# Optimization experiments

Hardware: AMD Instinct MI355X
Metric: run time of the kernel (lower is better)

Reference implementation:

```python
import jax, jax.numpy as jnp
import numpy as np

N, T, C, K = 32, 1024, 512, 64
EPS = 1e-12  # torch F.normalize eps


def _l2norm(v, axis):
    n = jnp.sqrt(jnp.sum(v * v, axis=axis, keepdims=True))
    return v / jnp.maximum(n, EPS)


def setup_inputs() -> dict:
    key = jax.random.key(0)
    k1, k2 = jax.random.split(key)
    x = jax.random.normal(k1, (N, T, C), dtype=jnp.float32)
    centroids = jax.random.uniform(k2, (K, C), dtype=jnp.float32)
    # mirrors _init_params: conv.weight = 0.2*centroids, conv.bias = -0.1*||centroids||
    W = 0.2 * centroids
    b = -0.1 * jnp.sqrt(jnp.sum(centroids * centroids, axis=1))
    return {"x": x, "W": W, "b": b, "centroids": centroids}


def reference(x, W, b, centroids):
    # x: [N, T, C] -> [N, C, T]
    xt = jnp.transpose(x, (0, 2, 1))
    # 1x1 Conv1d == per-timestep linear: logits [N, K, T]
    logits = jnp.einsum('kc,nct->nkt', W, xt) + b[None, :, None]
    a = jax.nn.softmax(logits, axis=1)  # softmax over clusters
    # vlad[n,k,c] = sum_t a[n,k,t] * (x[n,c,t] - centroid[k,c])
    #            = (a @ x^T) - sum_t(a) * centroid  (GEMM form, same math)
    vlad = jnp.einsum('nkt,nct->nkc', a, xt) - a.sum(axis=-1)[:, :, None] * centroids[None]
    vlad = _l2norm(vlad, axis=2)          # intra-normalization per cluster
    vlad = vlad.reshape(vlad.shape[0], -1)
    vlad = _l2norm(vlad, axis=1)          # global L2 normalization
    return vlad
```

## Files before the change

### kernel.cpp

```cpp
#include <hip/hip_runtime.h>
#include <cmath>

namespace {

constexpr int N = 32, T = 1024, C = 512, K = 64;
constexpr float EPS = 1e-12f;

typedef __attribute__((ext_vector_type(8))) short s8v;
typedef __attribute__((ext_vector_type(4))) short s4v;
typedef __attribute__((ext_vector_type(4))) float f4v;

__device__ inline unsigned short f2bh(float f) {
  __bf16 h = (__bf16)f;
  return __builtin_bit_cast(unsigned short, h);
}
__device__ inline float bh2f(unsigned short u) {
  __bf16 h = __builtin_bit_cast(__bf16, u);
  return (float)h;
}

#define MFMA16(A, B, Cc) __builtin_amdgcn_mfma_f32_16x16x32_bf16((A), (B), (Cc), 0, 0, 0)

__global__ __launch_bounds__(256) void k_prep(const float* __restrict__ W,
                                              unsigned short* __restrict__ Wh,
                                              unsigned short* __restrict__ Wl) {
  const int f = blockIdx.x * 256 + threadIdx.x;
  const float4 w = *(const float4*)&W[f * 4];
  float e[4] = {w.x, w.y, w.z, w.w};
  s4v h, l;
#pragma unroll
  for (int i = 0; i < 4; ++i) {
    unsigned short hb = f2bh(e[i]);
    h[i] = (short)hb;
    l[i] = (short)f2bh(e[i] - bh2f(hb));
  }
  *(s4v*)&Wh[f * 4] = h;
  *(s4v*)&Wl[f * 4] = l;
}

__global__ __launch_bounds__(512, 4) void k_gemm1(
    const float* __restrict__ x, const unsigned short* __restrict__ Wh,
    const unsigned short* __restrict__ Wl, const float* __restrict__ b,
    unsigned short* __restrict__ ath, unsigned short* __restrict__ atl,
    float* __restrict__ asum) {
  __shared__ __align__(16) unsigned short sm[4 * 64 * 72];
  __shared__ float asum_l[64];
  unsigned short* xh_s = sm;
  unsigned short* xl_s = sm + 64 * 72;
  unsigned short* wh_s = sm + 2 * 64 * 72;
  unsigned short* wl_s = sm + 3 * 64 * 72;

  const int tid = threadIdx.x;
  const int w = tid >> 6, lane = tid & 63, lm = lane & 15, lq = lane >> 4;
  const int tt = w >> 1;
  const int kh = w & 1;
  const long r0 = (long)blockIdx.x * 64;
  const int n = blockIdx.x >> 4;
  const int tl0 = (blockIdx.x & 15) * 64;

  if (tid < 64) asum_l[tid] = 0.f;

  f4v acc0 = {0.f, 0.f, 0.f, 0.f}, acc1 = {0.f, 0.f, 0.f, 0.f};
  const float bias0 = b[kh * 32 + lm], bias1 = b[kh * 32 + 16 + lm];

  for (int c0 = 0; c0 < C; c0 += 64) {
#pragma unroll
    for (int rr = 0; rr < 2; ++rr) {
      const int f = tid + rr * 512, t = f >> 4, cg = f & 15;
      const float4 xv = *(const float4*)&x[(r0 + t) * C + c0 + cg * 4];
      float e[4] = {xv.x, xv.y, xv.z, xv.w};
      s4v h, l;
#pragma unroll
      for (int i = 0; i < 4; ++i) {
        unsigned short hb = f2bh(e[i]);
        h[i] = (short)hb;
        l[i] = (short)f2bh(e[i] - bh2f(hb));
      }
      *(s4v*)&xh_s[t * 72 + cg * 4] = h;
      *(s4v*)&xl_s[t * 72 + cg * 4] = l;
    }
    {
      const int k = tid >> 3, u = tid & 7;
      *(s8v*)&wh_s[k * 72 + u * 8] = *(const s8v*)&Wh[k * C + c0 + u * 8];
      *(s8v*)&wl_s[k * 72 + u * 8] = *(const s8v*)&Wl[k * C + c0 + u * 8];
    }
    __syncthreads();

#pragma unroll
    for (int ks = 0; ks < 2; ++ks) {
      const int col = ks * 32 + lq * 8;
      const s8v ah = *(const s8v*)&xh_s[(tt * 16 + lm) * 72 + col];
      const s8v al = *(const s8v*)&xl_s[(tt * 16 + lm) * 72 + col];
      const s8v bh0 = *(const s8v*)&wh_s[(kh * 32 + lm) * 72 + col];
      const s8v bh1 = *(const s8v*)&wh_s[(kh * 32 + 16 + lm) * 72 + col];
      const s8v bl0 = *(const s8v*)&wl_s[(kh * 32 + lm) * 72 + col];
      const s8v bl1 = *(const s8v*)&wl_s[(kh * 32 + 16 + lm) * 72 + col];
      acc0 = MFMA16(ah, bh0, acc0);
      acc0 = MFMA16(ah, bl0, acc0);
      acc0 = MFMA16(al, bh0, acc0);
      acc1 = MFMA16(ah, bh1, acc1);
      acc1 = MFMA16(ah, bl1, acc1);
      acc1 = MFMA16(al, bh1, acc1);
    }
    __syncthreads();
  }

  float* Ls = (float*)sm;
  unsigned short* ath_l = sm + 8704;
  unsigned short* atl_l = sm + 8704 + 4864;
#pragma unroll
  for (int r = 0; r < 4; ++r) {
    Ls[(tt * 16 + lq * 4 + r) * 68 + kh * 32 + lm] = acc0[r] + bias0;
    Ls[(tt * 16 + lq * 4 + r) * 68 + kh * 32 + 16 + lm] = acc1[r] + bias1;
  }
  __syncthreads();

  {
    const int r = tid >> 3, j = tid & 7;
    const float4 v0 = *(const float4*)&Ls[r * 68 + j * 8];
    const float4 v1 = *(const float4*)&Ls[r * 68 + j * 8 + 4];
    float a[8] = {v0.x, v0.y, v0.z, v0.w, v1.x, v1.y, v1.z, v1.w};
    float m = a[0];
#pragma unroll
    for (int i = 1; i < 8; ++i) m = fmaxf(m, a[i]);
#pragma unroll
    for (int s = 1; s < 8; s <<= 1) m = fmaxf(m, __shfl_xor(m, s, 64));
    float sum = 0.f;
#pragma unroll
    for (int i = 0; i < 8; ++i) {
      a[i] = __expf(a[i] - m);
      sum += a[i];
    }
#pragma unroll
    for (int s = 1; s < 8; s <<= 1) sum += __shfl_xor(sum, s, 64);
    const float inv = 1.f / sum;
    float ps[8];
#pragma unroll
    for (int i = 0; i < 8; ++i) {
      a[i] *= inv;
      ps[i] = a[i];
    }
#pragma unroll
    for (int s = 8; s < 64; s <<= 1)
#pragma unroll
      for (int i = 0; i < 8; ++i) ps[i] += __shfl_xor(ps[i], s, 64);
    if ((tid & 56) == 0) {
#pragma unroll
      for (int i = 0; i < 8; ++i) atomicAdd(&asum_l[j * 8 + i], ps[i]);
    }
#pragma unroll
    for (int i = 0; i < 8; ++i) {
      const unsigned short hb = f2bh(a[i]);
      ath_l[(j * 8 + i) * 76 + r] = hb;
      atl_l[(j * 8 + i) * 76 + r] = f2bh(a[i] - bh2f(hb));
    }
  }
  __syncthreads();

  if (tid < 64) atomicAdd(&asum[n * K + tid], asum_l[tid]);
#pragma unroll
  for (int m = 0; m < 4; ++m) {
    const int idx = tid + m * 512;
    const int sel = idx >> 10, rem = idx & 1023, k = rem >> 4, uu = rem & 15;
    const unsigned short* src = sel ? atl_l : ath_l;
    unsigned short* dst = sel ? atl : ath;
    *(s4v*)&dst[((long)n * K + k) * T + tl0 + uu * 4] =
        *(const s4v*)&src[k * 76 + uu * 4];
  }
}

__global__ __launch_bounds__(256, 4) void k_gemm2(
    const float* __restrict__ x, const unsigned short* __restrict__ ath,
    const unsigned short* __restrict__ atl, float* __restrict__ part, int TS) {
  __shared__ __align__(16) unsigned short sm[4 * 64 * 72];
  unsigned short* ah_s = sm;
  unsigned short* al_s = sm + 4608;
  unsigned short* xh_s = sm + 9216;
  unsigned short* xl_s = sm + 13824;

  const int tid = threadIdx.x;
  const int w = tid >> 6, lane = tid & 63, lm = lane & 15, lq = lane >> 4;
  const int kh = w >> 1;
  const int ch = w & 1;
  const int bi = blockIdx.x;
  const int cchunk = bi & 7;
  const int tmp = bi >> 3;
  const int tchunk = tmp % TS, n = tmp / TS;
  const int c0 = cchunk * 64;
  const int tlen = T / TS;

  f4v acc[2][2] = {{{0.f, 0.f, 0.f, 0.f}, {0.f, 0.f, 0.f, 0.f}},
                   {{0.f, 0.f, 0.f, 0.f}, {0.f, 0.f, 0.f, 0.f}}};

  for (int t0 = tchunk * tlen; t0 < tchunk * tlen + tlen; t0 += 64) {
#pragma unroll
    for (int m = 0; m < 4; ++m) {
      const int idx = tid + m * 256;
      const int sel = idx >> 9, rem = idx & 511, k = rem >> 3, u = rem & 7;
      const unsigned short* src = sel ? atl : ath;
      unsigned short* dst = sel ? al_s : ah_s;
      *(s8v*)&dst[k * 72 + u * 8] =
          *(const s8v*)&src[((long)n * K + k) * T + t0 + u * 8];
    }
    {
      const int cg = tid & 15, tq = tid >> 4, t4 = tq * 4;
      float e[4][4];
#pragma unroll
      for (int i = 0; i < 4; ++i) {
        const float4 v =
            *(const float4*)&x[((long)n * T + t0 + t4 + i) * C + c0 + cg * 4];
        e[i][0] = v.x; e[i][1] = v.y; e[i][2] = v.z; e[i][3] = v.w;
      }
#pragma unroll
      for (int cc = 0; cc < 4; ++cc) {
        s4v h, l;
#pragma unroll
        for (int i = 0; i < 4; ++i) {
          unsigned short hb = f2bh(e[i][cc]);
          h[i] = (short)hb;
          l[i] = (short)f2bh(e[i][cc] - bh2f(hb));
        }
        *(s4v*)&xh_s[(cg * 4 + cc) * 72 + t4] = h;
        *(s4v*)&xl_s[(cg * 4 + cc) * 72 + t4] = l;
      }
    }
    __syncthreads();

#pragma unroll
    for (int ks = 0; ks < 2; ++ks) {
      const int col = ks * 32 + lq * 8;
      const s8v ah0 = *(const s8v*)&ah_s[(kh * 32 + lm) * 72 + col];
      const s8v ah1 = *(const s8v*)&ah_s[(kh * 32 + 16 + lm) * 72 + col];
      const s8v al0 = *(const s8v*)&al_s[(kh * 32 + lm) * 72 + col];
      const s8v al1 = *(const s8v*)&al_s[(kh * 32 + 16 + lm) * 72 + col];
      const s8v bh0 = *(const s8v*)&xh_s[(ch * 32 + lm) * 72 + col];
      const s8v bh1 = *(const s8v*)&xh_s[(ch * 32 + 16 + lm) * 72 + col];
      const s8v bl0 = *(const s8v*)&xl_s[(ch * 32 + lm) * 72 + col];
      const s8v bl1 = *(const s8v*)&xl_s[(ch * 32 + 16 + lm) * 72 + col];
      acc[0][0] = MFMA16(ah0, bh0, acc[0][0]);
      acc[0][0] = MFMA16(ah0, bl0, acc[0][0]);
      acc[0][0] = MFMA16(al0, bh0, acc[0][0]);
      acc[0][1] = MFMA16(ah0, bh1, acc[0][1]);
      acc[0][1] = MFMA16(ah0, bl1, acc[0][1]);
      acc[0][1] = MFMA16(al0, bh1, acc[0][1]);
      acc[1][0] = MFMA16(ah1, bh0, acc[1][0]);
      acc[1][0] = MFMA16(ah1, bl0, acc[1][0]);
      acc[1][0] = MFMA16(al1, bh0, acc[1][0]);
      acc[1][1] = MFMA16(ah1, bh1, acc[1][1]);
      acc[1][1] = MFMA16(ah1, bl1, acc[1][1]);
      acc[1][1] = MFMA16(al1, bh1, acc[1][1]);
    }
    __syncthreads();
  }

  float* pbase = part + ((long)tchunk * N + n) * K * C;
#pragma unroll
  for (int mt = 0; mt < 2; ++mt)
#pragma unroll
    for (int nt = 0; nt < 2; ++nt)
#pragma unroll
      for (int r = 0; r < 4; ++r) {
        const int k = kh * 32 + mt * 16 + lq * 4 + r;
        const int c = c0 + ch * 32 + nt * 16 + lm;
        pbase[(long)k * C + c] = acc[mt][nt][r];
      }
}

__global__ __launch_bounds__(128) void k_reduce(
    const float* __restrict__ part, const float* __restrict__ asum,
    const float* __restrict__ cent, float* __restrict__ vlad,
    float* __restrict__ sumsq, int TS) {
  __shared__ float r2[2];
  const int tid = threadIdx.x;
  const int n = blockIdx.x >> 6;
  const int k = blockIdx.x & 63;
  const int c = tid * 4;

  float4 v = {0.f, 0.f, 0.f, 0.f};
  for (int p = 0; p < TS; ++p) {
    const float4 pv =
        *(const float4*)&part[(((long)p * N + n) * K + k) * C + c];
    v.x += pv.x; v.y += pv.y; v.z += pv.z; v.w += pv.w;
  }
  const float as = asum[n * K + k];
  const float4 cv = *(const float4*)&cent[(long)k * C + c];
  v.x -= as * cv.x; v.y -= as * cv.y; v.z -= as * cv.z; v.w -= as * cv.w;
  *(float4*)&vlad[((long)n * K + k) * C + c] = v;

  float ss = v.x * v.x + v.y * v.y + v.z * v.z + v.w * v.w;
#pragma unroll
  for (int s = 1; s < 64; s <<= 1) ss += __shfl_xor(ss, s, 64);
  if ((tid & 63) == 0) r2[tid >> 6] = ss;
  __syncthreads();
  if (tid == 0) sumsq[n * K + k] = r2[0] + r2[1];
}

__global__ __launch_bounds__(256) void k_norm(
    const float* __restrict__ vlad, const float* __restrict__ sumsq,
    float* __restrict__ out) {
  __shared__ float denom[64];
  __shared__ float contrib[64];
  __shared__ float ginv;

  const int tid = threadIdx.x;
  const int n = blockIdx.x >> 4;
  const int chunk = blockIdx.x & 15;

  if (tid < 64) {
    const float ss = sumsq[n * K + tid];
    const float d = fmaxf(sqrtf(ss), EPS);
    denom[tid] = d;
    contrib[tid] = ss / (d * d);
  }
  __syncthreads();
  if (tid == 0) {
    float s = 0.f;
#pragma unroll
    for (int k = 0; k < K; ++k) s += contrib[k];
    ginv = 1.0f / fmaxf(sqrtf(s), EPS);
  }
  __syncthreads();

#pragma unroll
  for (int q = 0; q < 2; ++q) {
    const int f4 = tid + q * 256;
    const long off = chunk * 2048 + (long)f4 * 4;
    const int k = (int)(off >> 9);
    float4 v = *(const float4*)&vlad[(long)n * K * C + off];
    const float sc = ginv / denom[k];
    v.x *= sc; v.y *= sc; v.z *= sc; v.w *= sc;
    *(float4*)&out[(long)n * K * C + off] = v;
  }
}

}

extern "C" void kernel_launch(void* const* d_in, const int* in_sizes, int n_in,
                              void* d_out, int out_size, void* d_ws,
                              size_t ws_size, hipStream_t stream) {
  const float* x = reinterpret_cast<const float*>(d_in[0]);
  const float* W = reinterpret_cast<const float*>(d_in[1]);
  const float* b = reinterpret_cast<const float*>(d_in[2]);
  const float* cent = reinterpret_cast<const float*>(d_in[3]);
  float* out = reinterpret_cast<float*>(d_out);

  const size_t AT_BYTES = (size_t)N * K * T * 2;
  const size_t PART1 = (size_t)N * K * C * 4;
  const size_t W_BYTES = (size_t)K * C * 2;
  const size_t TAIL = 2 * W_BYTES + 2 * 8192;

  int TS = 4;
  while (TS > 1 && 2 * AT_BYTES + (size_t)TS * PART1 + TAIL > ws_size) TS >>= 1;

  char* p = (char*)d_ws;
  unsigned short* ath = (unsigned short*)p;        p += AT_BYTES;
  unsigned short* atl = (unsigned short*)p;        p += AT_BYTES;
  float* part = (float*)p;                         p += (size_t)TS * PART1;
  unsigned short* Wh = (unsigned short*)p;         p += W_BYTES;
  unsigned short* Wl = (unsigned short*)p;         p += W_BYTES;
  float* asum = (float*)p;                         p += 8192;
  float* sumsq = (float*)p;
  float* vlad = (float*)ath;

  hipMemsetAsync(asum, 0, (size_t)N * K * sizeof(float), stream);

  k_prep<<<32, 256, 0, stream>>>(W, Wh, Wl);
  k_gemm1<<<(N * T) / 64, 512, 0, stream>>>(x, Wh, Wl, b, ath, atl, asum);
  k_gemm2<<<N * TS * 8, 256, 0, stream>>>(x, ath, atl, part, TS);
  k_reduce<<<N * K, 128, 0, stream>>>(part, asum, cent, vlad, sumsq, TS);
  k_norm<<<N * 16, 256, 0, stream>>>(vlad, sumsq, out);
}
```

Before: 146.4 us.

## Restructure VLAD GEMMs with register prefetch, larger tiles, and fp32 assignment buffer

Removes the W pre-split kernel and the memset. gemm1 now splits W into bf16 hi/lo parts inline, and its 256 threads each compute 2x2 MFMA tiles. Both GEMMs prefetch the next global tile into registers while the current one is converted and computed. The soft-assignment is stored once as fp32 and split in gemm2, whose tile grows to 64x128 (fewer blocks, launch bound of 2). Cluster sums go to per-block partial buffers reduced in k_reduce instead of atomics; this trades more register pressure and lower occupancy for fewer launches, fewer syncs and more operand reuse.

```diff
diff --git a/kernel.cpp b/kernel.cpp
--- a/kernel.cpp
+++ b/kernel.cpp
@@ -6,9 +6,9 @@
 constexpr int N = 32, T = 1024, C = 512, K = 64;
 constexpr float EPS = 1e-12f;
 
-typedef __attribute__((ext_vector_type(8))) short s8v;
-typedef __attribute__((ext_vector_type(4))) short s4v;
-typedef __attribute__((ext_vector_type(4))) float f4v;
+typedef short s8v __attribute__((ext_vector_type(8)));
+typedef short s4v __attribute__((ext_vector_type(4)));
+typedef float f4v __attribute__((ext_vector_type(4)));
 
 __device__ inline unsigned short f2bh(float f) {
   __bf16 h = (__bf16)f;
@@ -21,30 +21,12 @@
 
 #define MFMA16(A, B, Cc) __builtin_amdgcn_mfma_f32_16x16x32_bf16((A), (B), (Cc), 0, 0, 0)
 
-__global__ __launch_bounds__(256) void k_prep(const float* __restrict__ W,
-                                              unsigned short* __restrict__ Wh,
-                                              unsigned short* __restrict__ Wl) {
-  const int f = blockIdx.x * 256 + threadIdx.x;
-  const float4 w = *(const float4*)&W[f * 4];
-  float e[4] = {w.x, w.y, w.z, w.w};
-  s4v h, l;
-#pragma unroll
-  for (int i = 0; i < 4; ++i) {
-    unsigned short hb = f2bh(e[i]);
-    h[i] = (short)hb;
-    l[i] = (short)f2bh(e[i] - bh2f(hb));
-  }
-  *(s4v*)&Wh[f * 4] = h;
-  *(s4v*)&Wl[f * 4] = l;
-}
-
-__global__ __launch_bounds__(512, 4) void k_gemm1(
-    const float* __restrict__ x, const unsigned short* __restrict__ Wh,
-    const unsigned short* __restrict__ Wl, const float* __restrict__ b,
-    unsigned short* __restrict__ ath, unsigned short* __restrict__ atl,
-    float* __restrict__ asum) {
+__global__ __launch_bounds__(256, 4) void k_gemm1(
+    const float* __restrict__ x, const float* __restrict__ W,
+    const float* __restrict__ b, float* __restrict__ aT,
+    float* __restrict__ asum_part) {
   __shared__ __align__(16) unsigned short sm[4 * 64 * 72];
-  __shared__ float asum_l[64];
+  __shared__ float asum_l[256];
   unsigned short* xh_s = sm;
   unsigned short* xl_s = sm + 64 * 72;
   unsigned short* wh_s = sm + 2 * 64 * 72;
@@ -52,163 +34,195 @@
 
   const int tid = threadIdx.x;
   const int w = tid >> 6, lane = tid & 63, lm = lane & 15, lq = lane >> 4;
-  const int tt = w >> 1;
+  const int th = w >> 1;
   const int kh = w & 1;
   const long r0 = (long)blockIdx.x * 64;
-  const int n = blockIdx.x >> 4;
-  const int tl0 = (blockIdx.x & 15) * 64;
-
-  if (tid < 64) asum_l[tid] = 0.f;
-
-  f4v acc0 = {0.f, 0.f, 0.f, 0.f}, acc1 = {0.f, 0.f, 0.f, 0.f};
-  const float bias0 = b[kh * 32 + lm], bias1 = b[kh * 32 + 16 + lm];
+  const int n = blockIdx.x >> 4, tl = blockIdx.x & 15;
+
+  f4v acc[2][2] = {};
+  float4 px[4], pw[4];
+#pragma unroll
+  for (int r = 0; r < 4; ++r) {
+    const int f = tid + r * 256, t = f >> 4, cg = f & 15;
+    px[r] = *(const float4*)&x[(r0 + t) * C + cg * 4];
+    pw[r] = *(const float4*)&W[(long)t * C + cg * 4];
+  }
 
   for (int c0 = 0; c0 < C; c0 += 64) {
-#pragma unroll
-    for (int rr = 0; rr < 2; ++rr) {
-      const int f = tid + rr * 512, t = f >> 4, cg = f & 15;
-      const float4 xv = *(const float4*)&x[(r0 + t) * C + c0 + cg * 4];
-      float e[4] = {xv.x, xv.y, xv.z, xv.w};
-      s4v h, l;
+    __syncthreads();
+#pragma unroll
+    for (int r = 0; r < 4; ++r) {
+      const int f = tid + r * 256, t = f >> 4, cg = f & 15;
+      const float ex[4] = {px[r].x, px[r].y, px[r].z, px[r].w};
+      const float ew[4] = {pw[r].x, pw[r].y, pw[r].z, pw[r].w};
+      s4v xh, xl, wh, wl;
 #pragma unroll
       for (int i = 0; i < 4; ++i) {
-        unsigned short hb = f2bh(e[i]);
-        h[i] = (short)hb;
-        l[i] = (short)f2bh(e[i] - bh2f(hb));
-      }
-      *(s4v*)&xh_s[t * 72 + cg * 4] = h;
-      *(s4v*)&xl_s[t * 72 + cg * 4] = l;
-    }
-    {
-      const int k = tid >> 3, u = tid & 7;
-      *(s8v*)&wh_s[k * 72 + u * 8] = *(const s8v*)&Wh[k * C + c0 + u * 8];
-      *(s8v*)&wl_s[k * 72 + u * 8] = *(const s8v*)&Wl[k * C + c0 + u * 8];
+        unsigned short hb = f2bh(ex[i]);
+        xh[i] = (short)hb; xl[i] = (short)f2bh(ex[i] - bh2f(hb));
+        hb = f2bh(ew[i]);
+        wh[i] = (short)hb; wl[i] = (short)f2bh(ew[i] - bh2f(hb));
+      }
+      *(s4v*)&xh_s[t * 72 + cg * 4] = xh;
+      *(s4v*)&xl_s[t * 72 + cg * 4] = xl;
+      *(s4v*)&wh_s[t * 72 + cg * 4] = wh;
+      *(s4v*)&wl_s[t * 72 + cg * 4] = wl;
+    }
+    if (c0 + 64 < C) {
+#pragma unroll
+      for (int r = 0; r < 4; ++r) {
+        const int f = tid + r * 256, t = f >> 4, cg = f & 15;
+        px[r] = *(const float4*)&x[(r0 + t) * C + c0 + 64 + cg * 4];
+        pw[r] = *(const float4*)&W[(long)t * C + c0 + 64 + cg * 4];
+      }
     }
     __syncthreads();
 
 #pragma unroll
     for (int ks = 0; ks < 2; ++ks) {
       const int col = ks * 32 + lq * 8;
-      const s8v ah = *(const s8v*)&xh_s[(tt * 16 + lm) * 72 + col];
-      const s8v al = *(const s8v*)&xl_s[(tt * 16 + lm) * 72 + col];
-      const s8v bh0 = *(const s8v*)&wh_s[(kh * 32 + lm) * 72 + col];
-      const s8v bh1 = *(const s8v*)&wh_s[(kh * 32 + 16 + lm) * 72 + col];
-      const s8v bl0 = *(const s8v*)&wl_s[(kh * 32 + lm) * 72 + col];
-      const s8v bl1 = *(const s8v*)&wl_s[(kh * 32 + 16 + lm) * 72 + col];
-      acc0 = MFMA16(ah, bh0, acc0);
-      acc0 = MFMA16(ah, bl0, acc0);
-      acc0 = MFMA16(al, bh0, acc0);
-      acc1 = MFMA16(ah, bh1, acc1);
-      acc1 = MFMA16(ah, bl1, acc1);
-      acc1 = MFMA16(al, bh1, acc1);
-    }
-    __syncthreads();
-  }
+      s8v ah[2], al[2], bh[2], bl[2];
+#pragma unroll
+      for (int i = 0; i < 2; ++i) {
+        ah[i] = *(const s8v*)&xh_s[(th * 32 + i * 16 + lm) * 72 + col];
+        al[i] = *(const s8v*)&xl_s[(th * 32 + i * 16 + lm) * 72 + col];
+        bh[i] = *(const s8v*)&wh_s[(kh * 32 + i * 16 + lm) * 72 + col];
+        bl[i] = *(const s8v*)&wl_s[(kh * 32 + i * 16 + lm) * 72 + col];
+      }
+#pragma unroll
+      for (int i = 0; i < 2; ++i)
+#pragma unroll
+        for (int j = 0; j < 2; ++j) {
+          acc[i][j] = MFMA16(ah[i], bh[j], acc[i][j]);
+          acc[i][j] = MFMA16(ah[i], bl[j], acc[i][j]);
+          acc[i][j] = MFMA16(al[i], bh[j], acc[i][j]);
+        }
+    }
+  }
+  __syncthreads();
 
   float* Ls = (float*)sm;
-  unsigned short* ath_l = sm + 8704;
-  unsigned short* atl_l = sm + 8704 + 4864;
+  float* Ls2 = (float*)(sm + 8704);
+  const float bias[2] = {b[kh * 32 + lm], b[kh * 32 + 16 + lm]};
+#pragma unroll
+  for (int i = 0; i < 2; ++i)
+#pragma unroll
+    for (int j = 0; j < 2; ++j)
+#pragma unroll
+      for (int r = 0; r < 4; ++r)
+        Ls[(th * 32 + i * 16 + lq * 4 + r) * 68 + kh * 32 + j * 16 + lm] =
+            acc[i][j][r] + bias[j];
+  __syncthreads();
+
+  {
+    const int row = tid >> 2, q = tid & 3;
+    float av[16];
+#pragma unroll
+    for (int u = 0; u < 4; ++u)
+      *(float4*)&av[u * 4] = *(const float4*)&Ls[row * 68 + q * 16 + u * 4];
+    float m = av[0];
+#pragma unroll
+    for (int i = 1; i < 16; ++i) m = fmaxf(m, av[i]);
+    m = fmaxf(m, __shfl_xor(m, 1, 64));
+    m = fmaxf(m, __shfl_xor(m, 2, 64));
+    float sum = 0.f;
+#pragma unroll
+    for (int i = 0; i < 16; ++i) {
+      av[i] = __expf(av[i] - m);
+      sum += av[i];
+    }
+    sum += __shfl_xor(sum, 1, 64);
+    sum += __shfl_xor(sum, 2, 64);
+    const float inv = 1.f / sum;
+    float ps[16];
+#pragma unroll
+    for (int i = 0; i < 16; ++i) {
+      av[i] *= inv;
+      ps[i] = av[i];
+      Ls2[(q * 16 + i) * 68 + row] = av[i];
+    }
+#pragma unroll
+    for (int s = 4; s < 64; s <<= 1)
+#pragma unroll
+      for (int i = 0; i < 16; ++i) ps[i] += __shfl_xor(ps[i], s, 64);
+    if (lane < 4) {
+#pragma unroll
+      for (int i = 0; i < 16; ++i) asum_l[w * 64 + q * 16 + i] = ps[i];
+    }
+  }
+  __syncthreads();
+
+  if (tid < 64) {
+    asum_part[(n * 16 + tl) * 64 + tid] = asum_l[tid] + asum_l[64 + tid] +
+                                          asum_l[128 + tid] + asum_l[192 + tid];
+  }
 #pragma unroll
   for (int r = 0; r < 4; ++r) {
-    Ls[(tt * 16 + lq * 4 + r) * 68 + kh * 32 + lm] = acc0[r] + bias0;
-    Ls[(tt * 16 + lq * 4 + r) * 68 + kh * 32 + 16 + lm] = acc1[r] + bias1;
-  }
-  __syncthreads();
-
-  {
-    const int r = tid >> 3, j = tid & 7;
-    const float4 v0 = *(const float4*)&Ls[r * 68 + j * 8];
-    const float4 v1 = *(const float4*)&Ls[r * 68 + j * 8 + 4];
-    float a[8] = {v0.x, v0.y, v0.z, v0.w, v1.x, v1.y, v1.z, v1.w};
-    float m = a[0];
-#pragma unroll
-    for (int i = 1; i < 8; ++i) m = fmaxf(m, a[i]);
-#pragma unroll
-    for (int s = 1; s < 8; s <<= 1) m = fmaxf(m, __shfl_xor(m, s, 64));
-    float sum = 0.f;
-#pragma unroll
-    for (int i = 0; i < 8; ++i) {
-      a[i] = __expf(a[i] - m);
-      sum += a[i];
-    }
-#pragma unroll
-    for (int s = 1; s < 8; s <<= 1) sum += __shfl_xor(sum, s, 64);
-    const float inv = 1.f / sum;
-    float ps[8];
-#pragma unroll
-    for (int i = 0; i < 8; ++i) {
-      a[i] *= inv;
-      ps[i] = a[i];
-    }
-#pragma unroll
-    for (int s = 8; s < 64; s <<= 1)
-#pragma unroll
-      for (int i = 0; i < 8; ++i) ps[i] += __shfl_xor(ps[i], s, 64);
-    if ((tid & 56) == 0) {
-#pragma unroll
-      for (int i = 0; i < 8; ++i) atomicAdd(&asum_l[j * 8 + i], ps[i]);
-    }
-#pragma unroll
-    for (int i = 0; i < 8; ++i) {
-      const unsigned short hb = f2bh(a[i]);
-      ath_l[(j * 8 + i) * 76 + r] = hb;
-      atl_l[(j * 8 + i) * 76 + r] = f2bh(a[i] - bh2f(hb));
-    }
-  }
-  __syncthreads();
-
-  if (tid < 64) atomicAdd(&asum[n * K + tid], asum_l[tid]);
-#pragma unroll
-  for (int m = 0; m < 4; ++m) {
-    const int idx = tid + m * 512;
-    const int sel = idx >> 10, rem = idx & 1023, k = rem >> 4, uu = rem & 15;
-    const unsigned short* src = sel ? atl_l : ath_l;
-    unsigned short* dst = sel ? atl : ath;
-    *(s4v*)&dst[((long)n * K + k) * T + tl0 + uu * 4] =
-        *(const s4v*)&src[k * 76 + uu * 4];
-  }
-}
-
-__global__ __launch_bounds__(256, 4) void k_gemm2(
-    const float* __restrict__ x, const unsigned short* __restrict__ ath,
-    const unsigned short* __restrict__ atl, float* __restrict__ part, int TS) {
-  __shared__ __align__(16) unsigned short sm[4 * 64 * 72];
+    const int u = tid + r * 256, k = u >> 4, tg = u & 15;
+    *(float4*)&aT[((long)n * K + k) * T + tl * 64 + tg * 4] =
+        *(const float4*)&Ls2[k * 68 + tg * 4];
+  }
+}
+
+__global__ __launch_bounds__(256, 2) void k_gemm2(
+    const float* __restrict__ x, const float* __restrict__ aT,
+    float* __restrict__ part, int TS) {
+  __shared__ __align__(16) unsigned short sm[(2 * 64 + 2 * 128) * 72];
   unsigned short* ah_s = sm;
-  unsigned short* al_s = sm + 4608;
-  unsigned short* xh_s = sm + 9216;
-  unsigned short* xl_s = sm + 13824;
+  unsigned short* al_s = sm + 64 * 72;
+  unsigned short* xh_s = sm + 2 * 64 * 72;
+  unsigned short* xl_s = sm + 2 * 64 * 72 + 128 * 72;
 
   const int tid = threadIdx.x;
   const int w = tid >> 6, lane = tid & 63, lm = lane & 15, lq = lane >> 4;
   const int kh = w >> 1;
   const int ch = w & 1;
   const int bi = blockIdx.x;
-  const int cchunk = bi & 7;
-  const int tmp = bi >> 3;
+  const int cchunk = bi & 3;
+  const int tmp = bi >> 2;
   const int tchunk = tmp % TS, n = tmp / TS;
-  const int c0 = cchunk * 64;
-  const int tlen = T / TS;
-
-  f4v acc[2][2] = {{{0.f, 0.f, 0.f, 0.f}, {0.f, 0.f, 0.f, 0.f}},
-                   {{0.f, 0.f, 0.f, 0.f}, {0.f, 0.f, 0.f, 0.f}}};
-
-  for (int t0 = tchunk * tlen; t0 < tchunk * tlen + tlen; t0 += 64) {
-#pragma unroll
-    for (int m = 0; m < 4; ++m) {
-      const int idx = tid + m * 256;
-      const int sel = idx >> 9, rem = idx & 511, k = rem >> 3, u = rem & 7;
-      const unsigned short* src = sel ? atl : ath;
-      unsigned short* dst = sel ? al_s : ah_s;
-      *(s8v*)&dst[k * 72 + u * 8] =
-          *(const s8v*)&src[((long)n * K + k) * T + t0 + u * 8];
-    }
-    {
-      const int cg = tid & 15, tq = tid >> 4, t4 = tq * 4;
+  const int c0 = cchunk * 128;
+  const int tlen = T / TS, tbase = tchunk * tlen;
+
+  f4v acc[2][4] = {};
+  float4 pa[4];
+#pragma unroll
+  for (int r = 0; r < 4; ++r) {
+    const int u = tid + r * 256, k = u >> 4, tg = u & 15;
+    pa[r] = *(const float4*)&aT[((long)n * K + k) * T + tbase + tg * 4];
+  }
+
+  for (int t0 = tbase; t0 < tbase + tlen; t0 += 64) {
+    __syncthreads();
+#pragma unroll
+    for (int r = 0; r < 4; ++r) {
+      const int u = tid + r * 256, k = u >> 4, tg = u & 15;
+      const float e[4] = {pa[r].x, pa[r].y, pa[r].z, pa[r].w};
+      s4v h, l;
+#pragma unroll
+      for (int i = 0; i < 4; ++i) {
+        unsigned short hb = f2bh(e[i]);
+        h[i] = (short)hb;
+        l[i] = (short)f2bh(e[i] - bh2f(hb));
+      }
+      *(s4v*)&ah_s[k * 72 + tg * 4] = h;
+      *(s4v*)&al_s[k * 72 + tg * 4] = l;
+    }
+    if (t0 + 64 < tbase + tlen) {
+#pragma unroll
+      for (int r = 0; r < 4; ++r) {
+        const int u = tid + r * 256, k = u >> 4, tg = u & 15;
+        pa[r] = *(const float4*)&aT[((long)n * K + k) * T + t0 + 64 + tg * 4];
+      }
+    }
+#pragma unroll
+    for (int r = 0; r < 2; ++r) {
+      const int u = tid + r * 256, cg = u & 31, tq = u >> 5;
       float e[4][4];
 #pragma unroll
       for (int i = 0; i < 4; ++i) {
         const float4 v =
-            *(const float4*)&x[((long)n * T + t0 + t4 + i) * C + c0 + cg * 4];
+            *(const float4*)&x[((long)n * T + t0 + tq * 4 + i) * C + c0 + cg * 4];
         e[i][0] = v.x; e[i][1] = v.y; e[i][2] = v.z; e[i][3] = v.w;
       }
 #pragma unroll
@@ -220,8 +234,8 @@
           h[i] = (short)hb;
           l[i] = (short)f2bh(e[i][cc] - bh2f(hb));
         }
-        *(s4v*)&xh_s[(cg * 4 + cc) * 72 + t4] = h;
-        *(s4v*)&xl_s[(cg * 4 + cc) * 72 + t4] = l;
+        *(s4v*)&xh_s[(cg * 4 + cc) * 72 + tq * 4] = h;
+        *(s4v*)&xl_s[(cg * 4 + cc) * 72 + tq * 4] = l;
       }
     }
     __syncthreads();
@@ -229,45 +243,41 @@
 #pragma unroll
     for (int ks = 0; ks < 2; ++ks) {
       const int col = ks * 32 + lq * 8;
-      const s8v ah0 = *(const s8v*)&ah_s[(kh * 32 + lm) * 72 + col];
-      const s8v ah1 = *(const s8v*)&ah_s[(kh * 32 + 16 + lm) * 72 + col];
-      const s8v al0 = *(const s8v*)&al_s[(kh * 32 + lm) * 72 + col];
-      const s8v al1 = *(const s8v*)&al_s[(kh * 32 + 16 + lm) * 72 + col];
-      const s8v bh0 = *(const s8v*)&xh_s[(ch * 32 + lm) * 72 + col];
-      const s8v bh1 = *(const s8v*)&xh_s[(ch * 32 + 16 + lm) * 72 + col];
-      const s8v bl0 = *(const s8v*)&xl_s[(ch * 32 + lm) * 72 + col];
-      const s8v bl1 = *(const s8v*)&xl_s[(ch * 32 + 16 + lm) * 72 + col];
-      acc[0][0] = MFMA16(ah0, bh0, acc[0][0]);
-      acc[0][0] = MFMA16(ah0, bl0, acc[0][0]);
-      acc[0][0] = MFMA16(al0, bh0, acc[0][0]);
-      acc[0][1] = MFMA16(ah0, bh1, acc[0][1]);
-      acc[0][1] = MFMA16(ah0, bl1, acc[0][1]);
-      acc[0][1] = MFMA16(al0, bh1, acc[0][1]);
-      acc[1][0] = MFMA16(ah1, bh0, acc[1][0]);
-      acc[1][0] = MFMA16(ah1, bl0, acc[1][0]);
-      acc[1][0] = MFMA16(al1, bh0, acc[1][0]);
-      acc[1][1] = MFMA16(ah1, bh1, acc[1][1]);
-      acc[1][1] = MFMA16(ah1, bl1, acc[1][1]);
-      acc[1][1] = MFMA16(al1, bh1, acc[1][1]);
-    }
-    __syncthreads();
-  }
-
-  float* pbase = part + ((long)tchunk * N + n) * K * C;
-#pragma unroll
-  for (int mt = 0; mt < 2; ++mt)
-#pragma unroll
-    for (int nt = 0; nt < 2; ++nt)
+      s8v ah[2], al[2];
+#pragma unroll
+      for (int i = 0; i < 2; ++i) {
+        ah[i] = *(const s8v*)&ah_s[(kh * 32 + i * 16 + lm) * 72 + col];
+        al[i] = *(const s8v*)&al_s[(kh * 32 + i * 16 + lm) * 72 + col];
+      }
+#pragma unroll
+      for (int j = 0; j < 4; ++j) {
+        const s8v bh = *(const s8v*)&xh_s[(ch * 64 + j * 16 + lm) * 72 + col];
+        const s8v bl = *(const s8v*)&xl_s[(ch * 64 + j * 16 + lm) * 72 + col];
+#pragma unroll
+        for (int i = 0; i < 2; ++i) {
+          acc[i][j] = MFMA16(ah[i], bh, acc[i][j]);
+          acc[i][j] = MFMA16(ah[i], bl, acc[i][j]);
+          acc[i][j] = MFMA16(al[i], bh, acc[i][j]);
+        }
+      }
+    }
+  }
+
+  float* pb = part + ((long)tchunk * N + n) * K * C;
+#pragma unroll
+  for (int i = 0; i < 2; ++i)
+#pragma unroll
+    for (int j = 0; j < 4; ++j)
 #pragma unroll
       for (int r = 0; r < 4; ++r) {
-        const int k = kh * 32 + mt * 16 + lq * 4 + r;
-        const int c = c0 + ch * 32 + nt * 16 + lm;
-        pbase[(long)k * C + c] = acc[mt][nt][r];
+        const int k = kh * 32 + i * 16 + lq * 4 + r;
+        const int c = c0 + ch * 64 + j * 16 + lm;
+        pb[(long)k * C + c] = acc[i][j][r];
       }
 }
 
 __global__ __launch_bounds__(128) void k_reduce(
-    const float* __restrict__ part, const float* __restrict__ asum,
+    const float* __restrict__ part, const float* __restrict__ asum_part,
     const float* __restrict__ cent, float* __restrict__ vlad,
     float* __restrict__ sumsq, int TS) {
   __shared__ float r2[2];
@@ -276,13 +286,15 @@
   const int k = blockIdx.x & 63;
   const int c = tid * 4;
 
+  float as = 0.f;
+#pragma unroll
+  for (int tl = 0; tl < 16; ++tl) as += asum_part[(n * 16 + tl) * 64 + k];
+
   float4 v = {0.f, 0.f, 0.f, 0.f};
   for (int p = 0; p < TS; ++p) {
-    const float4 pv =
-        *(const float4*)&part[(((long)p * N + n) * K + k) * C + c];
+    const float4 pv = *(const float4*)&part[(((long)p * N + n) * K + k) * C + c];
     v.x += pv.x; v.y += pv.y; v.z += pv.z; v.w += pv.w;
   }
-  const float as = asum[n * K + k];
   const float4 cv = *(const float4*)&cent[(long)k * C + c];
   v.x -= as * cv.x; v.y -= as * cv.y; v.z -= as * cv.z; v.w -= as * cv.w;
   *(float4*)&vlad[((long)n * K + k) * C + c] = v;
@@ -344,29 +356,22 @@
   const float* cent = reinterpret_cast<const float*>(d_in[3]);
   float* out = reinterpret_cast<float*>(d_out);
 
-  const size_t AT_BYTES = (size_t)N * K * T * 2;
+  const size_t AT_BYTES = (size_t)N * K * T * 4;
   const size_t PART1 = (size_t)N * K * C * 4;
-  const size_t W_BYTES = (size_t)K * C * 2;
-  const size_t TAIL = 2 * W_BYTES + 2 * 8192;
+  const size_t TAIL = 512 * 64 * 4 + 8192;
 
   int TS = 4;
-  while (TS > 1 && 2 * AT_BYTES + (size_t)TS * PART1 + TAIL > ws_size) TS >>= 1;
+  while (TS > 1 && AT_BYTES + (size_t)TS * PART1 + TAIL > ws_size) TS >>= 1;
 
   char* p = (char*)d_ws;
-  unsigned short* ath = (unsigned short*)p;        p += AT_BYTES;
-  unsigned short* atl = (unsigned short*)p;        p += AT_BYTES;
-  float* part = (float*)p;                         p += (size_t)TS * PART1;
-  unsigned short* Wh = (unsigned short*)p;         p += W_BYTES;
-  unsigned short* Wl = (unsigned short*)p;         p += W_BYTES;
-  float* asum = (float*)p;                         p += 8192;
+  float* aTg = (float*)p;                p += AT_BYTES;
+  float* part = (float*)p;               p += (size_t)TS * PART1;
+  float* asum_part = (float*)p;          p += 512 * 64 * 4;
   float* sumsq = (float*)p;
-  float* vlad = (float*)ath;
-
-  hipMemsetAsync(asum, 0, (size_t)N * K * sizeof(float), stream);
-
-  k_prep<<<32, 256, 0, stream>>>(W, Wh, Wl);
-  k_gemm1<<<(N * T) / 64, 512, 0, stream>>>(x, Wh, Wl, b, ath, atl, asum);
-  k_gemm2<<<N * TS * 8, 256, 0, stream>>>(x, ath, atl, part, TS);
-  k_reduce<<<N * K, 128, 0, stream>>>(part, asum, cent, vlad, sumsq, TS);
+  float* vlad = aTg;
+
+  k_gemm1<<<(N * T) / 64, 256, 0, stream>>>(x, W, b, aTg, asum_part);
+  k_gemm2<<<N * TS * 4, 256, 0, stream>>>(x, aTg, part, TS);
+  k_reduce<<<N * K, 128, 0, stream>>>(part, asum_part, cent, vlad, sumsq, TS);
   k_norm<<<N * 16, 256, 0, stream>>>(vlad, sumsq, out);
 }
```

Measured after the change: 133.2 us. 9.0% less time.
